# Kernel tuning notes

Hardware: AMD Instinct MI355X
Metric: run time of the kernel (lower is better)

The kernel has to match this reference:

```python
import jax, jax.numpy as jnp
import numpy as np
import math

L, R, B, S, D = 103, 512, 2, 512, 768


def setup_inputs() -> dict:
    key = jax.random.key(0)
    ks = jax.random.split(key, 16)
    n = lambda k, sh, s=1.0: jax.random.normal(k, sh, jnp.float32) * s
    W = 0.02  # weight init scale keeps softmax logits well-conditioned
    return {
        "output": n(ks[0], (B, S, D)),              # BERT sequence output (backbone treated as feature extractor)
        "attention_mask": jnp.ones((B, S), jnp.int32),
        "laws": n(ks[1], (L, R, D)),                # precomputed law representations (laws_rep.pkl)
        "Wq": n(ks[2], (D, D), W), "bq": jnp.zeros((D,), jnp.float32),
        "Wk": n(ks[3], (D, D), W), "bk": jnp.zeros((D,), jnp.float32),
        "Wv": n(ks[4], (D, D), W), "bv": jnp.zeros((D,), jnp.float32),
        "w_law_d": n(ks[5], (D,), W), "b_law_d": jnp.zeros((1,), jnp.float32),
        "w_law1": n(ks[6], (R,), W), "b_law1": jnp.zeros((1,), jnp.float32),
        "w_accu_d": n(ks[7], (D,), W), "b_accu_d": jnp.zeros((1,), jnp.float32),
        "w_accu1": n(ks[8], (R,), W), "b_accu1": jnp.zeros((1,), jnp.float32),
        "W_accu2": n(ks[9], (119, L), W), "b_accu2": jnp.zeros((119,), jnp.float32),
        "w_term_d": n(ks[10], (D,), W), "b_term_d": jnp.zeros((1,), jnp.float32),
        "w_term1": n(ks[11], (R,), W), "b_term1": jnp.zeros((1,), jnp.float32),
        "W_term2": n(ks[12], (11, L), W), "b_term2": jnp.zeros((11,), jnp.float32),
    }


def _forward(output, mask_f, laws, Wq, bq, Wk, bk, Wv, bv,
             w_law_d, b_law_d, w_law1, b_law1,
             w_accu_d, b_accu_d, w_accu1, b_accu1, W_accu2, b_accu2,
             w_term_d, b_term_d, w_term1, b_term1, W_term2, b_term2):
    laws_q = laws @ Wq + bq          # [L,R,D]
    facts_k = output @ Wk + bk       # [B,S,D]
    facts_v = output @ Wv + bv       # [B,S,D]
    # relevance: [L,B,R,S]
    scores = jnp.einsum('lrd,bsd->lbrs', laws_q, facts_k) / math.sqrt(768)
    scores = scores + (1.0 - mask_f)[None, :, None, :] * -10000.0
    probs = jax.nn.softmax(scores, axis=-1)          # (dropout omitted: eval mode)
    a_facts = jnp.einsum('lbrs,bsd->lbrd', probs, facts_v)
    g = jnp.transpose(a_facts, (1, 0, 2, 3))         # [B,L,R,D]
    act = jnp.tanh
    # law head: law1(tanh(law_d(g)))  -> [B,L]
    law = act(jnp.einsum('blrd,d->blr', g, w_law_d) + b_law_d)
    law = jnp.einsum('blr,r->bl', law, w_law1) + b_law1
    # accu head: accu2(tanh(accu1(tanh(accu_d(g))))) -> [B,119]
    accu = act(jnp.einsum('blrd,d->blr', g, w_accu_d) + b_accu_d)
    accu = act(jnp.einsum('blr,r->bl', accu, w_accu1) + b_accu1)
    accu = accu @ W_accu2.T + b_accu2
    # term head -> [B,11]
    term = act(jnp.einsum('blrd,d->blr', g, w_term_d) + b_term_d)
    term = act(jnp.einsum('blr,r->bl', term, w_term1) + b_term1)
    term = term @ W_term2.T + b_term2
    return law, accu, term


def reference(output, attention_mask, laws, Wq, bq, Wk, bk, Wv, bv,
              w_law_d, b_law_d, w_law1, b_law1,
              w_accu_d, b_accu_d, w_accu1, b_accu1, W_accu2, b_accu2,
              w_term_d, b_term_d, w_term1, b_term1, W_term2, b_term2):
    mask_f = attention_mask.astype(jnp.float32)
    return _forward(output, mask_f, laws, Wq, bq, Wk, bk, Wv, bv,
                    w_law_d, b_law_d, w_law1, b_law1,
                    w_accu_d, b_accu_d, w_accu1, b_accu1, W_accu2, b_accu2,
                    w_term_d, b_term_d, w_term1, b_term1, W_term2, b_term2)
```

## Files before the change

kernel.cpp:

```cpp
#include <hip/hip_runtime.h>

static constexpr int nL = 103, nR = 512, nB = 2, nS = 512, nD = 768;
static constexpr float INV_SQRT_D = 0.03608439182435161f;

typedef short bf16x8 __attribute__((ext_vector_type(8)));
typedef float f32x4 __attribute__((ext_vector_type(4)));
typedef unsigned short u16;
typedef unsigned short ushort4v __attribute__((ext_vector_type(4)));
typedef unsigned short ushort8v __attribute__((ext_vector_type(8)));

static constexpr size_t OFF_OUTB = 0;
static constexpr size_t OFF_MBF  = 393216;
static constexpr size_t OFF_KQB  = 688128;
static constexpr size_t OFF_QBK  = 1081344;
static constexpr size_t OFF_WKBQ = OFF_QBK + 768;
static constexpr size_t OFF_WV3  = OFF_WKBQ + 768;
static constexpr size_t OFF_CST  = OFF_WV3 + 2304;
static constexpr size_t OFF_C    = OFF_CST + 4;
static constexpr size_t OFF_HV   = OFF_C + 1024;
static constexpr size_t OFF_SUM  = OFF_HV + 3072;

__device__ inline float wredsum(float v) {
#pragma unroll
  for (int o = 32; o; o >>= 1) v += __shfl_xor(v, o);
  return v;
}

__device__ inline u16 f2bf(float f) {
  unsigned u = __builtin_bit_cast(unsigned, f);
  u += 0x7FFFu + ((u >> 16) & 1u);
  return (u16)(u >> 16);
}

__device__ inline bf16x8 cvt8(float4 a, float4 b) {
  ushort8v u;
  u[0]=f2bf(a.x); u[1]=f2bf(a.y); u[2]=f2bf(a.z); u[3]=f2bf(a.w);
  u[4]=f2bf(b.x); u[5]=f2bf(b.y); u[6]=f2bf(b.z); u[7]=f2bf(b.w);
  return __builtin_bit_cast(bf16x8, u);
}

__global__ __launch_bounds__(256) void k_prep(
    const float* __restrict__ Wq, const float* __restrict__ Wk,
    const float* __restrict__ Wv, const float* __restrict__ bq,
    const float* __restrict__ bk, const float* __restrict__ bv,
    const float* __restrict__ wld, const float* __restrict__ wad,
    const float* __restrict__ wtd, const float* __restrict__ outp,
    float* __restrict__ ws) {
  int tid = threadIdx.x, lane = tid & 63, w = tid >> 6;
  int bid = blockIdx.x;
  if (bid < 192) {
    int row = bid * 4 + w;
    const float* wqr = Wq + (size_t)row * nD;
    const float* wkr = Wk + (size_t)row * nD;
    const float* wvr = Wv + (size_t)row * nD;
    float dq = 0.f, dk = 0.f, d0 = 0.f, d1 = 0.f, d2 = 0.f;
#pragma unroll
    for (int k = 0; k < 3; ++k) {
      int off = lane * 4 + k * 256;
      float4 q4 = *(const float4*)(wqr + off);
      float4 k4 = *(const float4*)(wkr + off);
      float4 v4 = *(const float4*)(wvr + off);
      float4 bk4 = *(const float4*)(bk + off);
      float4 bq4 = *(const float4*)(bq + off);
      float4 l4 = *(const float4*)(wld + off);
      float4 a4 = *(const float4*)(wad + off);
      float4 t4 = *(const float4*)(wtd + off);
      dq += q4.x*bk4.x + q4.y*bk4.y + q4.z*bk4.z + q4.w*bk4.w;
      dk += k4.x*bq4.x + k4.y*bq4.y + k4.z*bq4.z + k4.w*bq4.w;
      d0 += v4.x*l4.x + v4.y*l4.y + v4.z*l4.z + v4.w*l4.w;
      d1 += v4.x*a4.x + v4.y*a4.y + v4.z*a4.z + v4.w*a4.w;
      d2 += v4.x*t4.x + v4.y*t4.y + v4.z*t4.z + v4.w*t4.w;
    }
    dq = wredsum(dq); dk = wredsum(dk);
    d0 = wredsum(d0); d1 = wredsum(d1); d2 = wredsum(d2);
    if (lane == 0) {
      ws[OFF_QBK + row] = dq;
      ws[OFF_WKBQ + row] = dk;
      ws[OFF_WV3 + row] = d0;
      ws[OFF_WV3 + 768 + row] = d1;
      ws[OFF_WV3 + 1536 + row] = d2;
    }
  } else if (bid == 192) {
    if (tid < 64) {
      float c0 = 0.f, c1 = 0.f, c2 = 0.f, c3 = 0.f;
      for (int j = lane; j < nD; j += 64) {
        c0 += bq[j]*bk[j]; c1 += bv[j]*wld[j]; c2 += bv[j]*wad[j]; c3 += bv[j]*wtd[j];
      }
      c0 = wredsum(c0); c1 = wredsum(c1); c2 = wredsum(c2); c3 = wredsum(c3);
      if (lane == 0) {
        ws[OFF_CST+0] = c0; ws[OFF_CST+1] = c1; ws[OFF_CST+2] = c2; ws[OFF_CST+3] = c3;
      }
    }
    for (int i = tid; i < 3 * nB * nL; i += 256) ws[OFF_SUM + i] = 0.f;
  } else {
    u16* outb = (u16*)(ws + OFF_OUTB);
    size_t e = ((size_t)(bid - 193) * 256 + tid) * 16;
    float4 f0 = *(const float4*)(outp + e);
    float4 f1 = *(const float4*)(outp + e + 4);
    float4 f2 = *(const float4*)(outp + e + 8);
    float4 f3 = *(const float4*)(outp + e + 12);
    *(ushort8v*)(outb + e)     = __builtin_bit_cast(ushort8v, cvt8(f0, f1));
    *(ushort8v*)(outb + e + 8) = __builtin_bit_cast(ushort8v, cvt8(f2, f3));
  }
}

__global__ __launch_bounds__(256) void k_mmM_chv(
    const float* __restrict__ Wq, const float* __restrict__ Wk,
    const float* __restrict__ outp, float* __restrict__ ws) {
  int tid = threadIdx.x, lane = tid & 63, w = tid >> 6;
  int bid = blockIdx.x;
  if (bid < 144) {
    u16* Mbf = (u16*)(ws + OFF_MBF);
    const int ti = bid / 12, tj = bid % 12;
    const int c4 = lane & 15, q4 = lane >> 4, wr = w >> 1, wc = w & 1;
    f32x4 acc[2][2];
#pragma unroll
    for (int i = 0; i < 2; ++i)
#pragma unroll
      for (int j = 0; j < 2; ++j) acc[i][j] = (f32x4){0.f,0.f,0.f,0.f};
    const float* Ab[2]; const float* Bb[2];
#pragma unroll
    for (int i = 0; i < 2; ++i)
      Ab[i] = Wq + (size_t)(ti*64 + wr*32 + i*16 + c4) * nD + q4*8;
#pragma unroll
    for (int j = 0; j < 2; ++j)
      Bb[j] = Wk + (size_t)(tj*64 + wc*32 + j*16 + c4) * nD + q4*8;
    for (int kt = 0; kt < 24; ++kt) {
      bf16x8 af[2], bf[2];
#pragma unroll
      for (int i = 0; i < 2; ++i)
        af[i] = cvt8(*(const float4*)(Ab[i] + kt*32), *(const float4*)(Ab[i] + kt*32 + 4));
#pragma unroll
      for (int j = 0; j < 2; ++j)
        bf[j] = cvt8(*(const float4*)(Bb[j] + kt*32), *(const float4*)(Bb[j] + kt*32 + 4));
#pragma unroll
      for (int i = 0; i < 2; ++i)
#pragma unroll
        for (int j = 0; j < 2; ++j)
          acc[i][j] = __builtin_amdgcn_mfma_f32_16x16x32_bf16(af[i], bf[j], acc[i][j], 0, 0, 0);
    }
#pragma unroll
    for (int i = 0; i < 2; ++i)
#pragma unroll
      for (int j = 0; j < 2; ++j) {
        int n = tj*64 + wc*32 + j*16 + c4;
#pragma unroll
        for (int reg = 0; reg < 4; ++reg) {
          int m = ti*64 + wr*32 + i*16 + q4*4 + reg;
          Mbf[(size_t)m * nD + n] = f2bf(acc[i][j][reg]);
        }
      }
  } else {
    int idx = (bid - 144) * 4 + w;
    const float* row = outp + (size_t)idx * nD;
    const float* wkbq = ws + OFF_WKBQ;
    const float* wv0 = ws + OFF_WV3;
    const float* wv1 = ws + OFF_WV3 + 768;
    const float* wv2 = ws + OFF_WV3 + 1536;
    float a0 = 0.f, a1 = 0.f, a2 = 0.f, a3 = 0.f;
#pragma unroll
    for (int k = 0; k < 3; ++k) {
      int off = lane * 4 + k * 256;
      float4 o4 = *(const float4*)(row + off);
      float4 k4 = *(const float4*)(wkbq + off);
      float4 l4 = *(const float4*)(wv0 + off);
      float4 c4v = *(const float4*)(wv1 + off);
      float4 t4 = *(const float4*)(wv2 + off);
      a0 += o4.x*k4.x + o4.y*k4.y + o4.z*k4.z + o4.w*k4.w;
      a1 += o4.x*l4.x + o4.y*l4.y + o4.z*l4.z + o4.w*l4.w;
      a2 += o4.x*c4v.x + o4.y*c4v.y + o4.z*c4v.z + o4.w*c4v.w;
      a3 += o4.x*t4.x + o4.y*t4.y + o4.z*t4.z + o4.w*t4.w;
    }
    a0 = wredsum(a0); a1 = wredsum(a1); a2 = wredsum(a2); a3 = wredsum(a3);
    if (lane == 0) {
      ws[OFF_C + idx]         = a0 + ws[OFF_CST+0];
      ws[OFF_HV + idx]        = a1 + ws[OFF_CST+1];
      ws[OFF_HV + 1024 + idx] = a2 + ws[OFF_CST+2];
      ws[OFF_HV + 2048 + idx] = a3 + ws[OFF_CST+3];
    }
  }
}

__global__ __launch_bounds__(256) void k_mkq(float* __restrict__ ws) {
  const u16* outb = (const u16*)(ws + OFF_OUTB);
  const u16* Mbf  = (const u16*)(ws + OFF_MBF);
  u16* kqB = (u16*)(ws + OFF_KQB);
  const float* qbk = ws + OFF_QBK;
  int tid = threadIdx.x, lane = tid & 63, w = tid >> 6;
  const int c4 = lane & 15, q4 = lane >> 4, wr = w >> 1, wc = w & 1;
  const int ti = blockIdx.y, tj = blockIdx.x;
  f32x4 acc[2][2];
#pragma unroll
  for (int i = 0; i < 2; ++i)
#pragma unroll
    for (int j = 0; j < 2; ++j) acc[i][j] = (f32x4){0.f,0.f,0.f,0.f};
  const u16* Ab[2]; const u16* Bb[2];
#pragma unroll
  for (int i = 0; i < 2; ++i)
    Ab[i] = outb + (size_t)(ti*64 + wr*32 + i*16 + c4) * nD + q4*8;
#pragma unroll
  for (int j = 0; j < 2; ++j)
    Bb[j] = Mbf + (size_t)(tj*64 + wc*32 + j*16 + c4) * nD + q4*8;
  for (int kt = 0; kt < 24; ++kt) {
    bf16x8 af[2], bf[2];
#pragma unroll
    for (int i = 0; i < 2; ++i) af[i] = *(const bf16x8*)(Ab[i] + kt*32);
#pragma unroll
    for (int j = 0; j < 2; ++j) bf[j] = *(const bf16x8*)(Bb[j] + kt*32);
#pragma unroll
    for (int i = 0; i < 2; ++i)
#pragma unroll
      for (int j = 0; j < 2; ++j)
        acc[i][j] = __builtin_amdgcn_mfma_f32_16x16x32_bf16(af[i], bf[j], acc[i][j], 0, 0, 0);
  }
#pragma unroll
  for (int i = 0; i < 2; ++i)
#pragma unroll
    for (int j = 0; j < 2; ++j) {
      int n = tj*64 + wc*32 + j*16 + c4;
      float bb = qbk[n];
#pragma unroll
      for (int reg = 0; reg < 4; ++reg) {
        int m = ti*64 + wr*32 + i*16 + q4*4 + reg;
        kqB[(((size_t)(n >> 3)) << 13) + ((size_t)m << 3) + (n & 7)] =
            f2bf(acc[i][j][reg] + bb);
      }
    }
}

__global__ __launch_bounds__(512) void k_attn(
    const float* __restrict__ laws, const u16* __restrict__ kqB,
    const int* __restrict__ mask, float* __restrict__ ws,
    const float* __restrict__ bld, const float* __restrict__ wl1,
    const float* __restrict__ bad, const float* __restrict__ wa1,
    const float* __restrict__ btd, const float* __restrict__ wt1) {
  __shared__ u16 Abuf[64 * 200];
  __shared__ f32x4 redS[8][64];
  const int tid = threadIdx.x, lane = tid & 63, w = tid >> 6;
  const int c4 = lane & 15, q4 = lane >> 4;
  const int b = blockIdx.x, rt8 = blockIdx.y, l = blockIdx.z;

  const int sr = tid >> 3, sq = tid & 7;
  const float* Asrc = laws + ((size_t)l * nR + rt8 * 64 + sr) * nD + sq * 4;
  u16* Aw = &Abuf[sr * 200 + sq * 4];

  const u16* Bbase = kqB + ((size_t)q4 * 1024 + (size_t)b * nS + w * 64 + c4) * 8;

  f32x4 acc[4][4];
#pragma unroll
  for (int rt = 0; rt < 4; ++rt)
#pragma unroll
    for (int ct = 0; ct < 4; ++ct) acc[rt][ct] = (f32x4){0.f,0.f,0.f,0.f};

  float4 g[6];
#pragma unroll
  for (int i = 0; i < 6; ++i) g[i] = *(const float4*)(Asrc + i * 32);
#pragma unroll
  for (int i = 0; i < 6; ++i) {
    ushort4v u;
    u[0]=f2bf(g[i].x); u[1]=f2bf(g[i].y); u[2]=f2bf(g[i].z); u[3]=f2bf(g[i].w);
    *(ushort4v*)(Aw + i * 32) = u;
  }
  __syncthreads();

#pragma unroll
  for (int s = 0; s < 4; ++s) {
    if (s < 3) {
#pragma unroll
      for (int i = 0; i < 6; ++i)
        g[i] = *(const float4*)(Asrc + (s + 1) * 192 + i * 32);
    }
#pragma unroll
    for (int k6 = 0; k6 < 6; ++k6) {
      const int kt = s * 6 + k6;
      bf16x8 bf[4];
#pragma unroll
      for (int ct = 0; ct < 4; ++ct)
        bf[ct] = *(const bf16x8*)(Bbase + (size_t)kt * 32768 + ct * 128);
      bf16x8 af[4];
#pragma unroll
      for (int rt = 0; rt < 4; ++rt)
        af[rt] = *(const bf16x8*)&Abuf[(rt * 16 + c4) * 200 + k6 * 32 + q4 * 8];
#pragma unroll
      for (int rt = 0; rt < 4; ++rt)
#pragma unroll
        for (int ct = 0; ct < 4; ++ct)
          acc[rt][ct] = __builtin_amdgcn_mfma_f32_16x16x32_bf16(af[rt], bf[ct],
                                                                acc[rt][ct], 0, 0, 0);
    }
    __syncthreads();
    if (s < 3) {
#pragma unroll
      for (int i = 0; i < 6; ++i) {
        ushort4v u;
        u[0]=f2bf(g[i].x); u[1]=f2bf(g[i].y); u[2]=f2bf(g[i].z); u[3]=f2bf(g[i].w);
        *(ushort4v*)(Aw + i * 32) = u;
      }
      __syncthreads();
    }
  }

  const float* cp  = ws + OFF_C + (size_t)b * nS;
  const float* hlp = ws + OFF_HV + (size_t)b * nS;
  const float* hap = ws + OFF_HV + 1024 + (size_t)b * nS;
  const float* htp = ws + OFF_HV + 2048 + (size_t)b * nS;
  float cc[4], hl[4], ha[4], ht[4], ma[4];
#pragma unroll
  for (int ct = 0; ct < 4; ++ct) {
    int s = w * 64 + ct * 16 + c4;
    cc[ct] = cp[s]; hl[ct] = hlp[s]; ha[ct] = hap[s]; ht[ct] = htp[s];
    ma[ct] = (1.0f - (float)mask[b * nS + s]) * -10000.0f;
  }

#pragma unroll
  for (int rt = 0; rt < 4; ++rt) {
#pragma unroll
    for (int reg = 0; reg < 4; ++reg) {
      float sse = 0.f, spl = 0.f, spa = 0.f, spt = 0.f;
#pragma unroll
      for (int ct = 0; ct < 4; ++ct) {
        float x = (acc[rt][ct][reg] + cc[ct]) * INV_SQRT_D + ma[ct];
        float e = __expf(x);
        sse += e; spl += e * hl[ct]; spa += e * ha[ct]; spt += e * ht[ct];
      }
#pragma unroll
      for (int o = 1; o < 16; o <<= 1) {
        sse += __shfl_xor(sse, o);
        spl += __shfl_xor(spl, o);
        spa += __shfl_xor(spa, o);
        spt += __shfl_xor(spt, o);
      }
      if (c4 == 0)
        redS[w][rt * 16 + q4 * 4 + reg] = (f32x4){sse, spl, spa, spt};
    }
  }
  __syncthreads();

  if (w == 0) {
    int row = lane;
    f32x4 t = (f32x4){0.f,0.f,0.f,0.f};
#pragma unroll
    for (int wc = 0; wc < 8; ++wc) t += redS[wc][row];
    float inv = 1.0f / t[0];
    int r = rt8 * 64 + row;
    float cl = tanhf(t[1] * inv + bld[0]) * wl1[r];
    float ca = tanhf(t[2] * inv + bad[0]) * wa1[r];
    float ctv = tanhf(t[3] * inv + btd[0]) * wt1[r];
#pragma unroll
    for (int o = 1; o < 64; o <<= 1) {
      cl += __shfl_xor(cl, o);
      ca += __shfl_xor(ca, o);
      ctv += __shfl_xor(ctv, o);
    }
    if (lane == 0) {
      float* sums = ws + OFF_SUM;
      atomicAdd(&sums[b * nL + l], cl);
      atomicAdd(&sums[nB * nL + b * nL + l], ca);
      atomicAdd(&sums[2 * nB * nL + b * nL + l], ctv);
    }
  }
}

__global__ void k_final(const float* __restrict__ ws, float* __restrict__ out,
                        const float* __restrict__ bl1, const float* __restrict__ ba1,
                        const float* __restrict__ Wa2, const float* __restrict__ ba2,
                        const float* __restrict__ bt1, const float* __restrict__ Wt2,
                        const float* __restrict__ bt2) {
  __shared__ float abl[nB * nL], tbl[nB * nL];
  int t = threadIdx.x;
  const float* sl = ws + OFF_SUM;
  const float* sa = sl + nB * nL;
  const float* st = sa + nB * nL;
  if (t < nB * nL) {
    out[t] = sl[t] + bl1[0];
    abl[t] = tanhf(sa[t] + ba1[0]);
    tbl[t] = tanhf(st[t] + bt1[0]);
  }
  __syncthreads();
  for (int idx = t; idx < nB * 119; idx += 256) {
    int b = idx / 119, j = idx % 119;
    float a = ba2[j];
    for (int ll = 0; ll < nL; ++ll) a += Wa2[j * nL + ll] * abl[b * nL + ll];
    out[nB * nL + idx] = a;
  }
  for (int idx = t; idx < nB * 11; idx += 256) {
    int b = idx / 11, j = idx % 11;
    float a = bt2[j];
    for (int ll = 0; ll < nL; ++ll) a += Wt2[j * nL + ll] * tbl[b * nL + ll];
    out[nB * nL + nB * 119 + idx] = a;
  }
}

extern "C" void kernel_launch(void* const* d_in, const int* in_sizes, int n_in,
                              void* d_out, int out_size, void* d_ws, size_t ws_size,
                              hipStream_t stream) {
  (void)in_sizes; (void)n_in; (void)out_size; (void)ws_size;
  const float* outp = (const float*)d_in[0];
  const int*   mask = (const int*)d_in[1];
  const float* laws = (const float*)d_in[2];
  const float* Wq = (const float*)d_in[3];  const float* bq = (const float*)d_in[4];
  const float* Wk = (const float*)d_in[5];  const float* bk = (const float*)d_in[6];
  const float* Wv = (const float*)d_in[7];  const float* bv = (const float*)d_in[8];
  const float* wld = (const float*)d_in[9];  const float* bld = (const float*)d_in[10];
  const float* wl1 = (const float*)d_in[11]; const float* bl1 = (const float*)d_in[12];
  const float* wad = (const float*)d_in[13]; const float* bad = (const float*)d_in[14];
  const float* wa1 = (const float*)d_in[15]; const float* ba1 = (const float*)d_in[16];
  const float* Wa2 = (const float*)d_in[17]; const float* ba2 = (const float*)d_in[18];
  const float* wtd = (const float*)d_in[19]; const float* btd = (const float*)d_in[20];
  const float* wt1 = (const float*)d_in[21]; const float* bt1 = (const float*)d_in[22];
  const float* Wt2 = (const float*)d_in[23]; const float* bt2 = (const float*)d_in[24];
  float* ws = (float*)d_ws;
  float* fout = (float*)d_out;
  u16* kqB = (u16*)(ws + OFF_KQB);

  k_prep<<<385, 256, 0, stream>>>(Wq, Wk, Wv, bq, bk, bv, wld, wad, wtd, outp, ws);
  k_mmM_chv<<<400, 256, 0, stream>>>(Wq, Wk, outp, ws);
  k_mkq<<<dim3(12, 16), 256, 0, stream>>>(ws);
  k_attn<<<dim3(nB, 8, nL), 512, 0, stream>>>(laws, kqB, mask, ws,
                                              bld, wl1, bad, wa1, btd, wt1);
  k_final<<<1, 256, 0, stream>>>(ws, fout, bl1, ba1, Wa2, ba2, bt1, Wt2, bt2);
}
```

Before: 459.9 us.

## Double-buffer the laws LDS tile in k_attn and split prefetch into halves

k_attn's bf16 copy of the laws tile in shared memory becomes a two-slot ping-pong buffer, so the next stage's conversion and store can overlap the current stage's MFMAs. This removes one __syncthreads per stage. The global prefetch is split into two halves of three float4 loads each to cut register pressure, and A fragments are loaded per row tile instead of all at once. It also adds a launch-bounds occupancy hint of 4 and doubles the Abuf footprint, which may limit how many blocks fit per CU.

```diff
diff --git a/kernel.cpp b/kernel.cpp
--- a/kernel.cpp
+++ b/kernel.cpp
@@ -228,13 +228,13 @@
     }
 }
 
-__global__ __launch_bounds__(512) void k_attn(
+__global__ __launch_bounds__(512, 4) void k_attn(
     const float* __restrict__ laws, const u16* __restrict__ kqB,
     const int* __restrict__ mask, float* __restrict__ ws,
     const float* __restrict__ bld, const float* __restrict__ wl1,
     const float* __restrict__ bad, const float* __restrict__ wa1,
     const float* __restrict__ btd, const float* __restrict__ wt1) {
-  __shared__ u16 Abuf[64 * 200];
+  __shared__ u16 Abuf[2][64 * 200];
   __shared__ f32x4 redS[8][64];
   const int tid = threadIdx.x, lane = tid & 63, w = tid >> 6;
   const int c4 = lane & 15, q4 = lane >> 4;
@@ -242,62 +242,90 @@
 
   const int sr = tid >> 3, sq = tid & 7;
   const float* Asrc = laws + ((size_t)l * nR + rt8 * 64 + sr) * nD + sq * 4;
-  u16* Aw = &Abuf[sr * 200 + sq * 4];
+  const int awo = sr * 200 + sq * 4;
 
   const u16* Bbase = kqB + ((size_t)q4 * 1024 + (size_t)b * nS + w * 64 + c4) * 8;
 
+  float4 g[6];
+#pragma unroll
+  for (int i = 0; i < 6; ++i) g[i] = *(const float4*)(Asrc + i * 32);
+
   f32x4 acc[4][4];
 #pragma unroll
   for (int rt = 0; rt < 4; ++rt)
 #pragma unroll
     for (int ct = 0; ct < 4; ++ct) acc[rt][ct] = (f32x4){0.f,0.f,0.f,0.f};
 
-  float4 g[6];
-#pragma unroll
-  for (int i = 0; i < 6; ++i) g[i] = *(const float4*)(Asrc + i * 32);
 #pragma unroll
   for (int i = 0; i < 6; ++i) {
     ushort4v u;
     u[0]=f2bf(g[i].x); u[1]=f2bf(g[i].y); u[2]=f2bf(g[i].z); u[3]=f2bf(g[i].w);
-    *(ushort4v*)(Aw + i * 32) = u;
+    *(ushort4v*)(&Abuf[0][0] + awo + i * 32) = u;
   }
   __syncthreads();
 
 #pragma unroll
   for (int s = 0; s < 4; ++s) {
+    const u16* cur = &Abuf[s & 1][0];
+    u16* nxt = &Abuf[(s & 1) ^ 1][0];
+    float4 gA[3], gB[3];
     if (s < 3) {
 #pragma unroll
-      for (int i = 0; i < 6; ++i)
-        g[i] = *(const float4*)(Asrc + (s + 1) * 192 + i * 32);
-    }
-#pragma unroll
-    for (int k6 = 0; k6 < 6; ++k6) {
-      const int kt = s * 6 + k6;
+      for (int i = 0; i < 3; ++i)
+        gA[i] = *(const float4*)(Asrc + (s + 1) * 192 + i * 32);
+    }
+#pragma unroll
+    for (int kk = 0; kk < 3; ++kk) {
+      const int kt = s * 6 + kk;
       bf16x8 bf[4];
 #pragma unroll
       for (int ct = 0; ct < 4; ++ct)
         bf[ct] = *(const bf16x8*)(Bbase + (size_t)kt * 32768 + ct * 128);
-      bf16x8 af[4];
-#pragma unroll
-      for (int rt = 0; rt < 4; ++rt)
-        af[rt] = *(const bf16x8*)&Abuf[(rt * 16 + c4) * 200 + k6 * 32 + q4 * 8];
-#pragma unroll
-      for (int rt = 0; rt < 4; ++rt)
+#pragma unroll
+      for (int rt = 0; rt < 4; ++rt) {
+        bf16x8 af = *(const bf16x8*)&cur[(rt * 16 + c4) * 200 + kk * 32 + q4 * 8];
 #pragma unroll
         for (int ct = 0; ct < 4; ++ct)
-          acc[rt][ct] = __builtin_amdgcn_mfma_f32_16x16x32_bf16(af[rt], bf[ct],
+          acc[rt][ct] = __builtin_amdgcn_mfma_f32_16x16x32_bf16(af, bf[ct],
                                                                 acc[rt][ct], 0, 0, 0);
+      }
+    }
+    if (s < 3) {
+#pragma unroll
+      for (int i = 0; i < 3; ++i) {
+        ushort4v u;
+        u[0]=f2bf(gA[i].x); u[1]=f2bf(gA[i].y); u[2]=f2bf(gA[i].z); u[3]=f2bf(gA[i].w);
+        *(ushort4v*)(nxt + awo + i * 32) = u;
+      }
+#pragma unroll
+      for (int i = 0; i < 3; ++i)
+        gB[i] = *(const float4*)(Asrc + (s + 1) * 192 + (i + 3) * 32);
+    }
+#pragma unroll
+    for (int kk = 3; kk < 6; ++kk) {
+      const int kt = s * 6 + kk;
+      bf16x8 bf[4];
+#pragma unroll
+      for (int ct = 0; ct < 4; ++ct)
+        bf[ct] = *(const bf16x8*)(Bbase + (size_t)kt * 32768 + ct * 128);
+#pragma unroll
+      for (int rt = 0; rt < 4; ++rt) {
+        bf16x8 af = *(const bf16x8*)&cur[(rt * 16 + c4) * 200 + kk * 32 + q4 * 8];
+#pragma unroll
+        for (int ct = 0; ct < 4; ++ct)
+          acc[rt][ct] = __builtin_amdgcn_mfma_f32_16x16x32_bf16(af, bf[ct],
+                                                                acc[rt][ct], 0, 0, 0);
+      }
+    }
+    if (s < 3) {
+#pragma unroll
+      for (int i = 0; i < 3; ++i) {
+        ushort4v u;
+        u[0]=f2bf(gB[i].x); u[1]=f2bf(gB[i].y); u[2]=f2bf(gB[i].z); u[3]=f2bf(gB[i].w);
+        *(ushort4v*)(nxt + awo + (i + 3) * 32) = u;
+      }
     }
     __syncthreads();
-    if (s < 3) {
-#pragma unroll
-      for (int i = 0; i < 6; ++i) {
-        ushort4v u;
-        u[0]=f2bf(g[i].x); u[1]=f2bf(g[i].y); u[2]=f2bf(g[i].z); u[3]=f2bf(g[i].w);
-        *(ushort4v*)(Aw + i * 32) = u;
-      }
-      __syncthreads();
-    }
   }
 
   const float* cp  = ws + OFF_C + (size_t)b * nS;
```

After: 426.7 us. 1.08x faster.

## Double-buffer laws tile in attention kernel and merge prep kernels

Applied to the files above, without the earlier changes.

The attention kernel now uses two LDS buffers for the converted laws tile and interleaves the global loads and bf16 stores for the next stage with the MFMA work on the current stage. This removes one barrier per stage and shortens the live range of the prefetch registers. The Wq·Wk^T product moves into the prep kernel, and the kq product merges with the c/hv reductions, so the launch count drops from five to four. It also adds launch_bounds(512,4) to k_attn, which may force register spilling, and doubles the LDS footprint per block.

```diff
diff --git a/kernel.cpp b/kernel.cpp
--- a/kernel.cpp
+++ b/kernel.cpp
@@ -39,7 +39,13 @@
   return __builtin_bit_cast(bf16x8, u);
 }
 
-__global__ __launch_bounds__(256) void k_prep(
+__device__ inline void st4(u16* dst, float4 g) {
+  ushort4v u;
+  u[0]=f2bf(g.x); u[1]=f2bf(g.y); u[2]=f2bf(g.z); u[3]=f2bf(g.w);
+  *(ushort4v*)dst = u;
+}
+
+__global__ __launch_bounds__(256) void k_prep_mm(
     const float* __restrict__ Wq, const float* __restrict__ Wk,
     const float* __restrict__ Wv, const float* __restrict__ bq,
     const float* __restrict__ bk, const float* __restrict__ bv,
@@ -92,7 +98,7 @@
       }
     }
     for (int i = tid; i < 3 * nB * nL; i += 256) ws[OFF_SUM + i] = 0.f;
-  } else {
+  } else if (bid < 385) {
     u16* outb = (u16*)(ws + OFF_OUTB);
     size_t e = ((size_t)(bid - 193) * 256 + tid) * 16;
     float4 f0 = *(const float4*)(outp + e);
@@ -101,17 +107,10 @@
     float4 f3 = *(const float4*)(outp + e + 12);
     *(ushort8v*)(outb + e)     = __builtin_bit_cast(ushort8v, cvt8(f0, f1));
     *(ushort8v*)(outb + e + 8) = __builtin_bit_cast(ushort8v, cvt8(f2, f3));
-  }
-}
-
-__global__ __launch_bounds__(256) void k_mmM_chv(
-    const float* __restrict__ Wq, const float* __restrict__ Wk,
-    const float* __restrict__ outp, float* __restrict__ ws) {
-  int tid = threadIdx.x, lane = tid & 63, w = tid >> 6;
-  int bid = blockIdx.x;
-  if (bid < 144) {
+  } else {
     u16* Mbf = (u16*)(ws + OFF_MBF);
-    const int ti = bid / 12, tj = bid % 12;
+    const int mb = bid - 385;
+    const int ti = mb / 12, tj = mb % 12;
     const int c4 = lane & 15, q4 = lane >> 4, wr = w >> 1, wc = w & 1;
     f32x4 acc[2][2];
 #pragma unroll
@@ -150,8 +149,59 @@
           Mbf[(size_t)m * nD + n] = f2bf(acc[i][j][reg]);
         }
       }
+  }
+}
+
+__global__ __launch_bounds__(256) void k_mkq_chv(
+    const float* __restrict__ outp, float* __restrict__ ws) {
+  int tid = threadIdx.x, lane = tid & 63, w = tid >> 6;
+  int bid = blockIdx.x;
+  if (bid < 192) {
+    const u16* outb = (const u16*)(ws + OFF_OUTB);
+    const u16* Mbf  = (const u16*)(ws + OFF_MBF);
+    u16* kqB = (u16*)(ws + OFF_KQB);
+    const float* qbk = ws + OFF_QBK;
+    const int c4 = lane & 15, q4 = lane >> 4, wr = w >> 1, wc = w & 1;
+    const int ti = bid / 12, tj = bid % 12;
+    f32x4 acc[2][2];
+#pragma unroll
+    for (int i = 0; i < 2; ++i)
+#pragma unroll
+      for (int j = 0; j < 2; ++j) acc[i][j] = (f32x4){0.f,0.f,0.f,0.f};
+    const u16* Ab[2]; const u16* Bb[2];
+#pragma unroll
+    for (int i = 0; i < 2; ++i)
+      Ab[i] = outb + (size_t)(ti*64 + wr*32 + i*16 + c4) * nD + q4*8;
+#pragma unroll
+    for (int j = 0; j < 2; ++j)
+      Bb[j] = Mbf + (size_t)(tj*64 + wc*32 + j*16 + c4) * nD + q4*8;
+    for (int kt = 0; kt < 24; ++kt) {
+      bf16x8 af[2], bf[2];
+#pragma unroll
+      for (int i = 0; i < 2; ++i) af[i] = *(const bf16x8*)(Ab[i] + kt*32);
+#pragma unroll
+      for (int j = 0; j < 2; ++j) bf[j] = *(const bf16x8*)(Bb[j] + kt*32);
+#pragma unroll
+      for (int i = 0; i < 2; ++i)
+#pragma unroll
+        for (int j = 0; j < 2; ++j)
+          acc[i][j] = __builtin_amdgcn_mfma_f32_16x16x32_bf16(af[i], bf[j], acc[i][j], 0, 0, 0);
+    }
+#pragma unroll
+    for (int i = 0; i < 2; ++i)
+#pragma unroll
+      for (int j = 0; j < 2; ++j) {
+        int n = tj*64 + wc*32 + j*16 + c4;
+        float bb = qbk[n];
+#pragma unroll
+        for (int reg = 0; reg < 4; ++reg) {
+          int m = ti*64 + wr*32 + i*16 + q4*4 + reg;
+          kqB[(((size_t)(n >> 3)) << 13) + ((size_t)m << 3) + (n & 7)] =
+              f2bf(acc[i][j][reg] + bb);
+        }
+      }
   } else {
-    int idx = (bid - 144) * 4 + w;
+    int idx = (bid - 192) * 4 + w;
     const float* row = outp + (size_t)idx * nD;
     const float* wkbq = ws + OFF_WKBQ;
     const float* wv0 = ws + OFF_WV3;
@@ -181,60 +231,13 @@
   }
 }
 
-__global__ __launch_bounds__(256) void k_mkq(float* __restrict__ ws) {
-  const u16* outb = (const u16*)(ws + OFF_OUTB);
-  const u16* Mbf  = (const u16*)(ws + OFF_MBF);
-  u16* kqB = (u16*)(ws + OFF_KQB);
-  const float* qbk = ws + OFF_QBK;
-  int tid = threadIdx.x, lane = tid & 63, w = tid >> 6;
-  const int c4 = lane & 15, q4 = lane >> 4, wr = w >> 1, wc = w & 1;
-  const int ti = blockIdx.y, tj = blockIdx.x;
-  f32x4 acc[2][2];
-#pragma unroll
-  for (int i = 0; i < 2; ++i)
-#pragma unroll
-    for (int j = 0; j < 2; ++j) acc[i][j] = (f32x4){0.f,0.f,0.f,0.f};
-  const u16* Ab[2]; const u16* Bb[2];
-#pragma unroll
-  for (int i = 0; i < 2; ++i)
-    Ab[i] = outb + (size_t)(ti*64 + wr*32 + i*16 + c4) * nD + q4*8;
-#pragma unroll
-  for (int j = 0; j < 2; ++j)
-    Bb[j] = Mbf + (size_t)(tj*64 + wc*32 + j*16 + c4) * nD + q4*8;
-  for (int kt = 0; kt < 24; ++kt) {
-    bf16x8 af[2], bf[2];
-#pragma unroll
-    for (int i = 0; i < 2; ++i) af[i] = *(const bf16x8*)(Ab[i] + kt*32);
-#pragma unroll
-    for (int j = 0; j < 2; ++j) bf[j] = *(const bf16x8*)(Bb[j] + kt*32);
-#pragma unroll
-    for (int i = 0; i < 2; ++i)
-#pragma unroll
-      for (int j = 0; j < 2; ++j)
-        acc[i][j] = __builtin_amdgcn_mfma_f32_16x16x32_bf16(af[i], bf[j], acc[i][j], 0, 0, 0);
-  }
-#pragma unroll
-  for (int i = 0; i < 2; ++i)
-#pragma unroll
-    for (int j = 0; j < 2; ++j) {
-      int n = tj*64 + wc*32 + j*16 + c4;
-      float bb = qbk[n];
-#pragma unroll
-      for (int reg = 0; reg < 4; ++reg) {
-        int m = ti*64 + wr*32 + i*16 + q4*4 + reg;
-        kqB[(((size_t)(n >> 3)) << 13) + ((size_t)m << 3) + (n & 7)] =
-            f2bf(acc[i][j][reg] + bb);
-      }
-    }
-}
-
-__global__ __launch_bounds__(512) void k_attn(
+__global__ __launch_bounds__(512, 4) void k_attn(
     const float* __restrict__ laws, const u16* __restrict__ kqB,
     const int* __restrict__ mask, float* __restrict__ ws,
     const float* __restrict__ bld, const float* __restrict__ wl1,
     const float* __restrict__ bad, const float* __restrict__ wa1,
     const float* __restrict__ btd, const float* __restrict__ wt1) {
-  __shared__ u16 Abuf[64 * 200];
+  __shared__ u16 Abuf[2][64 * 200];
   __shared__ f32x4 redS[8][64];
   const int tid = threadIdx.x, lane = tid & 63, w = tid >> 6;
   const int c4 = lane & 15, q4 = lane >> 4;
@@ -242,7 +245,7 @@
 
   const int sr = tid >> 3, sq = tid & 7;
   const float* Asrc = laws + ((size_t)l * nR + rt8 * 64 + sr) * nD + sq * 4;
-  u16* Aw = &Abuf[sr * 200 + sq * 4];
+  const int awo = sr * 200 + sq * 4;
 
   const u16* Bbase = kqB + ((size_t)q4 * 1024 + (size_t)b * nS + w * 64 + c4) * 8;
 
@@ -252,53 +255,65 @@
 #pragma unroll
     for (int ct = 0; ct < 4; ++ct) acc[rt][ct] = (f32x4){0.f,0.f,0.f,0.f};
 
-  float4 g[6];
-#pragma unroll
-  for (int i = 0; i < 6; ++i) g[i] = *(const float4*)(Asrc + i * 32);
-#pragma unroll
-  for (int i = 0; i < 6; ++i) {
-    ushort4v u;
-    u[0]=f2bf(g[i].x); u[1]=f2bf(g[i].y); u[2]=f2bf(g[i].z); u[3]=f2bf(g[i].w);
-    *(ushort4v*)(Aw + i * 32) = u;
+#pragma unroll
+  for (int j = 0; j < 3; ++j) {
+    float4 p0 = *(const float4*)(Asrc + (2*j) * 32);
+    float4 p1 = *(const float4*)(Asrc + (2*j+1) * 32);
+    st4(&Abuf[0][0] + awo + (2*j) * 32, p0);
+    st4(&Abuf[0][0] + awo + (2*j+1) * 32, p1);
   }
   __syncthreads();
 
+#define COMPUTE_KK(CUR, KT, KK)                                               \
+  do {                                                                        \
+    bf16x8 bf0 = *(const bf16x8*)(Bbase + (size_t)(KT) * 32768 + 0 * 128);    \
+    bf16x8 bf1 = *(const bf16x8*)(Bbase + (size_t)(KT) * 32768 + 1 * 128);    \
+    bf16x8 bf2 = *(const bf16x8*)(Bbase + (size_t)(KT) * 32768 + 2 * 128);    \
+    bf16x8 bf3 = *(const bf16x8*)(Bbase + (size_t)(KT) * 32768 + 3 * 128);    \
+    _Pragma("unroll")                                                         \
+    for (int rt = 0; rt < 4; ++rt) {                                          \
+      bf16x8 af = *(const bf16x8*)&(CUR)[(rt * 16 + c4) * 200 + (KK) * 32 + q4 * 8]; \
+      acc[rt][0] = __builtin_amdgcn_mfma_f32_16x16x32_bf16(af, bf0, acc[rt][0], 0, 0, 0); \
+      acc[rt][1] = __builtin_amdgcn_mfma_f32_16x16x32_bf16(af, bf1, acc[rt][1], 0, 0, 0); \
+      acc[rt][2] = __builtin_amdgcn_mfma_f32_16x16x32_bf16(af, bf2, acc[rt][2], 0, 0, 0); \
+      acc[rt][3] = __builtin_amdgcn_mfma_f32_16x16x32_bf16(af, bf3, acc[rt][3], 0, 0, 0); \
+    }                                                                         \
+  } while (0)
+
 #pragma unroll
   for (int s = 0; s < 4; ++s) {
+    const u16* cur = &Abuf[s & 1][0];
+    u16* nxt = &Abuf[(s & 1) ^ 1][0];
+    float4 g0, g1;
     if (s < 3) {
-#pragma unroll
-      for (int i = 0; i < 6; ++i)
-        g[i] = *(const float4*)(Asrc + (s + 1) * 192 + i * 32);
-    }
-#pragma unroll
-    for (int k6 = 0; k6 < 6; ++k6) {
-      const int kt = s * 6 + k6;
-      bf16x8 bf[4];
-#pragma unroll
-      for (int ct = 0; ct < 4; ++ct)
-        bf[ct] = *(const bf16x8*)(Bbase + (size_t)kt * 32768 + ct * 128);
-      bf16x8 af[4];
-#pragma unroll
-      for (int rt = 0; rt < 4; ++rt)
-        af[rt] = *(const bf16x8*)&Abuf[(rt * 16 + c4) * 200 + k6 * 32 + q4 * 8];
-#pragma unroll
-      for (int rt = 0; rt < 4; ++rt)
-#pragma unroll
-        for (int ct = 0; ct < 4; ++ct)
-          acc[rt][ct] = __builtin_amdgcn_mfma_f32_16x16x32_bf16(af[rt], bf[ct],
-                                                                acc[rt][ct], 0, 0, 0);
+      g0 = *(const float4*)(Asrc + (s + 1) * 192 + 0 * 32);
+      g1 = *(const float4*)(Asrc + (s + 1) * 192 + 1 * 32);
+    }
+    COMPUTE_KK(cur, s * 6 + 0, 0);
+    COMPUTE_KK(cur, s * 6 + 1, 1);
+    if (s < 3) {
+      st4(nxt + awo + 0 * 32, g0);
+      st4(nxt + awo + 1 * 32, g1);
+      g0 = *(const float4*)(Asrc + (s + 1) * 192 + 2 * 32);
+      g1 = *(const float4*)(Asrc + (s + 1) * 192 + 3 * 32);
+    }
+    COMPUTE_KK(cur, s * 6 + 2, 2);
+    COMPUTE_KK(cur, s * 6 + 3, 3);
+    if (s < 3) {
+      st4(nxt + awo + 2 * 32, g0);
+      st4(nxt + awo + 3 * 32, g1);
+      g0 = *(const float4*)(Asrc + (s + 1) * 192 + 4 * 32);
+      g1 = *(const float4*)(Asrc + (s + 1) * 192 + 5 * 32);
+    }
+    COMPUTE_KK(cur, s * 6 + 4, 4);
+    COMPUTE_KK(cur, s * 6 + 5, 5);
+    if (s < 3) {
+      st4(nxt + awo + 4 * 32, g0);
+      st4(nxt + awo + 5 * 32, g1);
     }
     __syncthreads();
-    if (s < 3) {
-#pragma unroll
-      for (int i = 0; i < 6; ++i) {
-        ushort4v u;
-        u[0]=f2bf(g[i].x); u[1]=f2bf(g[i].y); u[2]=f2bf(g[i].z); u[3]=f2bf(g[i].w);
-        *(ushort4v*)(Aw + i * 32) = u;
-      }
-      __syncthreads();
-    }
-  }
+  }
+#undef COMPUTE_KK
 
   const float* cp  = ws + OFF_C + (size_t)b * nS;
   const float* hlp = ws + OFF_HV + (size_t)b * nS;
@@ -413,9 +428,8 @@
   float* fout = (float*)d_out;
   u16* kqB = (u16*)(ws + OFF_KQB);
 
-  k_prep<<<385, 256, 0, stream>>>(Wq, Wk, Wv, bq, bk, bv, wld, wad, wtd, outp, ws);
-  k_mmM_chv<<<400, 256, 0, stream>>>(Wq, Wk, outp, ws);
-  k_mkq<<<dim3(12, 16), 256, 0, stream>>>(ws);
+  k_prep_mm<<<529, 256, 0, stream>>>(Wq, Wk, Wv, bq, bk, bv, wld, wad, wtd, outp, ws);
+  k_mkq_chv<<<448, 256, 0, stream>>>(outp, ws);
   k_attn<<<dim3(nB, 8, nL), 512, 0, stream>>>(laws, kqB, mask, ws,
                                               bld, wl1, bad, wa1, btd, wt1);
   k_final<<<1, 256, 0, stream>>>(ws, fout, bl1, ba1, Wa2, ba2, bt1, Wt2, bt2);
```

After: 412.7 us. -10.3%, faster.
